# Performance work log

Measured on AMD Instinct MI355X. Metric: run time of the kernel, lower is better.

## Reference

```python
import jax, jax.numpy as jnp
import numpy as np

B, LC, LM, D = 128, 512, 512, 512

def setup_inputs() -> dict:
    key = jax.random.key(0)
    k1, k2, k3 = jax.random.split(key, 3)
    context = jax.random.normal(k1, (B, LC, D), dtype=jnp.float32)
    main = jax.random.normal(k2, (B, LM, D), dtype=jnp.float32)
    W = jax.random.normal(k3, (D, 1), dtype=jnp.float32)
    return {"context": context, "main": main, "W": W}

def reference(context, main, W):
    # scores[b,c,m] = <context[b,c,:], main[b,m,:]>
    scores = jnp.einsum('bcd,bmd->bcm', context, main)
    # softmax over last axis (main positions), matching K.softmax default axis=-1
    attn = jax.nn.softmax(scores, axis=-1)           # [B, LC, LM]
    # Keras dot(axes=1): contract context-position axis -> [B, LM, D]
    aligned = jnp.einsum('bcm,bcd->bmd', attn, context)
    diff = main - aligned                            # [B, LM, D]
    # project to scalar per main position, softmax over positions
    w = jax.nn.softmax(jnp.einsum('bmd,d->bm', diff, W[:, 0]), axis=-1)  # [B, LM]
    # weighted sum over main positions -> [B, D]
    out = jnp.einsum('bm,bmd->bd', w, diff)
    return out
```

## Files before the change

kernel.cpp:

```cpp
#include <hip/hip_runtime.h>

#define B_  128
#define LC_ 512
#define LM_ 512
#define D_  512

typedef __attribute__((ext_vector_type(8))) short short8;
typedef __attribute__((ext_vector_type(16))) float f32x16;
typedef unsigned int u32;

__device__ __forceinline__ unsigned short bf16_rn(float x) {
  unsigned u = __float_as_uint(x);
  unsigned r = u + 0x7fffu + ((u >> 16) & 1u);
  return (unsigned short)(r >> 16);
}
__device__ __forceinline__ float bf2f(short s) {
  return __uint_as_float((u32)(unsigned short)s << 16);
}
__device__ __forceinline__ void gl_lds16(const void* g, void* l) {
  __builtin_amdgcn_global_load_lds((const __attribute__((address_space(1))) u32*)g,
                                   (__attribute__((address_space(3))) u32*)l, 16, 0, 0);
}

#define CVT1(SRC, WS, AH, AL, IDX, ACCU)                         \
  { unsigned short hb_ = bf16_rn(SRC);                           \
    float hf_ = __uint_as_float((u32)hb_ << 16);                 \
    AH[IDX] = (short)hb_;                                        \
    AL[IDX] = (short)bf16_rn((SRC) - hf_);                       \
    ACCU = fmaf((SRC), (WS), ACCU); }

__global__ __launch_bounds__(256) void k_cvt_main(
    const float* __restrict__ mn, const float* __restrict__ W,
    short* __restrict__ BtH, short* __restrict__ BtL,
    float* __restrict__ v) {
  __shared__ float sW[512];
  int tid = threadIdx.x;
  sW[tid] = W[tid];
  sW[tid + 256] = W[tid + 256];
  __syncthreads();
  int wave = blockIdx.x * 4 + (tid >> 6);
  int b = wave >> 4, mt = wave & 15;
  int lane = tid & 63, rowl = lane & 31, h = lane >> 5;
  const float* src = mn + ((size_t)b * LM_ + 32 * mt + rowl) * D_ + 8 * h;
  float acc = 0.f;
  for (int ks = 0; ks < 32; ks++) {
    float4 f0 = *(const float4*)(src + 16 * ks);
    float4 f1 = *(const float4*)(src + 16 * ks + 4);
    int k = 16 * ks + 8 * h;
    float4 w0 = *(const float4*)&sW[k];
    float4 w1 = *(const float4*)&sW[k + 4];
    short8 vh, vl;
    CVT1(f0.x, w0.x, vh, vl, 0, acc); CVT1(f0.y, w0.y, vh, vl, 1, acc);
    CVT1(f0.z, w0.z, vh, vl, 2, acc); CVT1(f0.w, w0.w, vh, vl, 3, acc);
    CVT1(f1.x, w1.x, vh, vl, 4, acc); CVT1(f1.y, w1.y, vh, vl, 5, acc);
    CVT1(f1.z, w1.z, vh, vl, 6, acc); CVT1(f1.w, w1.w, vh, vl, 7, acc);
    size_t off = (((size_t)b * 32 + ks) * 16 + mt) * 512 + (size_t)lane * 8;
    *(short8*)(BtH + off) = vh;
    *(short8*)(BtL + off) = vl;
  }
  acc += __shfl_xor(acc, 32, 64);
  if (h == 0) v[b * LM_ + 32 * mt + rowl] = acc;
}

struct __align__(16) Smem3 {
  short8 Bf[2][2][16][64];
  short8 Af[2][2][4][64];
  float sW[512];
  float red[4][128];
  float cmb[128];
  float uld[128];
  float tpw[2][4][128];
};

__global__ __launch_bounds__(512, 2) void k_scores_mfma9(
    const float* __restrict__ ctx, const short* __restrict__ BtH,
    const short* __restrict__ BtL, const float* __restrict__ W,
    unsigned short* __restrict__ P16, float* __restrict__ tpart) {
  __shared__ Smem3 sm;
  int p = blockIdx.x;
  int b = (p & 7) | ((p >> 5) << 3);
  int cblk = (p >> 3) & 3;
  int c0 = cblk * 128;
  int tid = threadIdx.x;
  int lane = tid & 63, wv = tid >> 6;
  int rowl = lane & 31, h = lane >> 5;

  f32x16 acc[2][4];
  #pragma unroll
  for (int r = 0; r < 2; r++)
    #pragma unroll
    for (int mtl = 0; mtl < 4; mtl++)
      #pragma unroll
      for (int j = 0; j < 16; j++) acc[r][mtl][j] = 0.f;

  auto stageB = [&](int bf, int ks) {
    #pragma unroll
    for (int rep = 0; rep < 2; rep++) {
      int mt = wv + 8 * rep;
      size_t off = (((size_t)b * 32 + ks) * 16 + mt) * 512 + (size_t)lane * 8;
      gl_lds16(BtH + off, &sm.Bf[bf][0][mt][0]);
      gl_lds16(BtL + off, &sm.Bf[bf][1][mt][0]);
    }
  };
  auto cvtA = [&](int bf, int ks, const float4& g0, const float4& g1, float& au) {
    float xs[8] = {g0.x, g0.y, g0.z, g0.w, g1.x, g1.y, g1.z, g1.w};
    int k = 16 * ks + 8 * h;
    float4 w0 = *(const float4*)&sm.sW[k];
    float4 w1 = *(const float4*)&sm.sW[k + 4];
    float ws[8] = {w0.x, w0.y, w0.z, w0.w, w1.x, w1.y, w1.z, w1.w};
    short8 vh, vl;
    #pragma unroll
    for (int e = 0; e < 8; e++) {
      unsigned short hb = bf16_rn(xs[e]);
      float hf = __uint_as_float((unsigned)hb << 16);
      vh[e] = (short)hb;
      vl[e] = (short)bf16_rn(xs[e] - hf);
      au = fmaf(xs[e], ws[e], au);
    }
    *(short8*)&sm.Af[bf][0][wv][lane] = vh;
    *(short8*)&sm.Af[bf][1][wv][lane] = vl;
  };

  sm.sW[tid] = W[tid];
  float accu = 0.f;
  stageB(0, 0);
  const float* arow = ctx + ((size_t)b * LC_ + c0 + 32 * wv + rowl) * D_ + 8 * h;
  float4 g0, g1;
  if (wv < 4) {
    g0 = *(const float4*)(arow);
    g1 = *(const float4*)(arow + 4);
  }
  __syncthreads();
  if (wv < 4) cvtA(0, 0, g0, g1, accu);
  __syncthreads();

  for (int ks = 0; ks < 32; ks++) {
    int buf = ks & 1;
    if (ks < 31) {
      stageB(buf ^ 1, ks + 1);
      if (wv < 4) {
        const float* ap = arow + 16 * (ks + 1);
        g0 = *(const float4*)ap;
        g1 = *(const float4*)(ap + 4);
      }
    }
    int rt0 = (wv >> 2) * 2;
    short8 ah0 = sm.Af[buf][0][rt0][lane];
    short8 ah1 = sm.Af[buf][0][rt0 + 1][lane];
    short8 al0 = sm.Af[buf][1][rt0][lane];
    short8 al1 = sm.Af[buf][1][rt0 + 1][lane];
    #pragma unroll
    for (int mtl = 0; mtl < 4; mtl++) {
      int mtg = (wv & 3) * 4 + mtl;
      short8 bh = sm.Bf[buf][0][mtg][lane];
      short8 bl = sm.Bf[buf][1][mtg][lane];
      acc[0][mtl] = __builtin_amdgcn_mfma_f32_32x32x16_bf16(ah0, bh, acc[0][mtl], 0, 0, 0);
      acc[0][mtl] = __builtin_amdgcn_mfma_f32_32x32x16_bf16(ah0, bl, acc[0][mtl], 0, 0, 0);
      acc[0][mtl] = __builtin_amdgcn_mfma_f32_32x32x16_bf16(al0, bh, acc[0][mtl], 0, 0, 0);
      acc[1][mtl] = __builtin_amdgcn_mfma_f32_32x32x16_bf16(ah1, bh, acc[1][mtl], 0, 0, 0);
      acc[1][mtl] = __builtin_amdgcn_mfma_f32_32x32x16_bf16(ah1, bl, acc[1][mtl], 0, 0, 0);
      acc[1][mtl] = __builtin_amdgcn_mfma_f32_32x32x16_bf16(al1, bh, acc[1][mtl], 0, 0, 0);
    }
    if (ks < 31 && wv < 4) cvtA(buf ^ 1, ks + 1, g0, g1, accu);
    __syncthreads();
  }

  if (wv < 4) {
    accu += __shfl_xor(accu, 32, 64);
    if (h == 0) sm.uld[32 * wv + rowl] = accu;
  }

  #pragma unroll
  for (int r = 0; r < 2; r++)
    #pragma unroll
    for (int j = 0; j < 16; j++) {
      float mx = fmaxf(fmaxf(acc[r][0][j], acc[r][1][j]),
                       fmaxf(acc[r][2][j], acc[r][3][j]));
      #pragma unroll
      for (int s = 1; s <= 16; s <<= 1) mx = fmaxf(mx, __shfl_xor(mx, s, 64));
      if (rowl == 0)
        sm.red[wv & 3][64 * (wv >> 2) + 32 * r + (j & 3) + 8 * (j >> 2) + 4 * h] = mx;
    }
  __syncthreads();
  if (tid < 128)
    sm.cmb[tid] = fmaxf(fmaxf(sm.red[0][tid], sm.red[1][tid]),
                        fmaxf(sm.red[2][tid], sm.red[3][tid]));
  __syncthreads();
  #pragma unroll
  for (int r = 0; r < 2; r++)
    #pragma unroll
    for (int j = 0; j < 16; j++) {
      int row = 64 * (wv >> 2) + 32 * r + (j & 3) + 8 * (j >> 2) + 4 * h;
      float mx = sm.cmb[row];
      float s = 0.f;
      #pragma unroll
      for (int mtl = 0; mtl < 4; mtl++) {
        float e = __expf(acc[r][mtl][j] - mx);
        acc[r][mtl][j] = e;
        s += e;
      }
      #pragma unroll
      for (int st = 1; st <= 16; st <<= 1) s += __shfl_xor(s, st, 64);
      if (rowl == 0) sm.red[wv & 3][row] = s;
    }
  __syncthreads();
  if (tid < 128)
    sm.cmb[tid] = sm.red[0][tid] + sm.red[1][tid] + sm.red[2][tid] + sm.red[3][tid];
  __syncthreads();

  unsigned short* Pb = P16 + ((size_t)b * LC_ + c0) * LM_;
  float tp[4] = {0.f, 0.f, 0.f, 0.f};
  #pragma unroll
  for (int r = 0; r < 2; r++)
    #pragma unroll
    for (int j = 0; j < 16; j++) {
      int row = 64 * (wv >> 2) + 32 * r + (j & 3) + 8 * (j >> 2) + 4 * h;
      float rinv = 1.f / sm.cmb[row];
      float uu = sm.uld[row];
      #pragma unroll
      for (int mtl = 0; mtl < 4; mtl++) {
        float pv = acc[r][mtl][j] * rinv;
        Pb[(size_t)row * LM_ + 128 * (wv & 3) + 32 * mtl + rowl] = bf16_rn(pv);
        tp[mtl] = fmaf(pv, uu, tp[mtl]);
      }
    }
  #pragma unroll
  for (int mtl = 0; mtl < 4; mtl++) tp[mtl] += __shfl_xor(tp[mtl], 32, 64);
  if (h == 0) {
    #pragma unroll
    for (int mtl = 0; mtl < 4; mtl++)
      sm.tpw[wv >> 2][wv & 3][32 * mtl + rowl] = tp[mtl];
  }
  __syncthreads();
  {
    int m = tid;
    tpart[((size_t)b * 4 + cblk) * LM_ + m] =
        sm.tpw[0][m >> 7][m & 127] + sm.tpw[1][m >> 7][m & 127];
  }
}

__global__ __launch_bounds__(256) void k_tw(const float* __restrict__ tpart,
                                            const float* __restrict__ v,
                                            float* __restrict__ w_) {
  int b = blockIdx.x;
  int tid = threadIdx.x;
  int m0 = tid * 2;
  const float* tp = tpart + (size_t)b * 4 * LM_;
  float s0 = 0.f, s1 = 0.f;
  #pragma unroll
  for (int cb = 0; cb < 4; cb++) {
    s0 += tp[cb * LM_ + m0];
    s1 += tp[cb * LM_ + m0 + 1];
  }
  float x0 = v[b * LM_ + m0] - s0;
  float x1 = v[b * LM_ + m0 + 1] - s1;
  float mx = fmaxf(x0, x1);
  #pragma unroll
  for (int s = 32; s >= 1; s >>= 1) mx = fmaxf(mx, __shfl_xor(mx, s, 64));
  __shared__ float redm[4], reds[4];
  int wvv = tid >> 6, ln = tid & 63;
  if (ln == 0) redm[wvv] = mx;
  __syncthreads();
  mx = fmaxf(fmaxf(redm[0], redm[1]), fmaxf(redm[2], redm[3]));
  float e0 = __expf(x0 - mx), e1 = __expf(x1 - mx);
  float sum = e0 + e1;
  #pragma unroll
  for (int s = 32; s >= 1; s >>= 1) sum += __shfl_xor(sum, s, 64);
  if (ln == 0) reds[wvv] = sum;
  __syncthreads();
  sum = reds[0] + reds[1] + reds[2] + reds[3];
  float rinv = 1.0f / sum;
  float2 o; o.x = e0 * rinv; o.y = e1 * rinv;
  *(float2*)&w_[b * LM_ + m0] = o;
}

__global__ __launch_bounds__(256) void k_q(const unsigned short* __restrict__ P16,
                                           const float* __restrict__ w,
                                           float* __restrict__ q) {
  int b = blockIdx.y;
  int c0 = blockIdx.x * 32;
  int wvv = threadIdx.x >> 6, ln = threadIdx.x & 63;
  __shared__ float sw[LM_];
  *(float2*)&sw[threadIdx.x * 2] = *(const float2*)&w[b * LM_ + threadIdx.x * 2];
  __syncthreads();
  #pragma unroll
  for (int rr = 0; rr < 8; rr++) {
    int c = c0 + wvv * 8 + rr;
    short8 pv = *((const short8*)(P16 + ((size_t)b * LC_ + c) * LM_) + ln);
    float4 w0 = *(const float4*)&sw[ln * 8];
    float4 w1 = *(const float4*)&sw[ln * 8 + 4];
    float acc = bf2f(pv[0]) * w0.x + bf2f(pv[1]) * w0.y
              + bf2f(pv[2]) * w0.z + bf2f(pv[3]) * w0.w
              + bf2f(pv[4]) * w1.x + bf2f(pv[5]) * w1.y
              + bf2f(pv[6]) * w1.z + bf2f(pv[7]) * w1.w;
    #pragma unroll
    for (int s = 32; s >= 1; s >>= 1) acc += __shfl_xor(acc, s, 64);
    if (ln == 0) q[b * LC_ + c] = acc;
  }
}

__global__ __launch_bounds__(256) void k_out(const float* __restrict__ ctx,
                                             const short* __restrict__ BtH,
                                             const short* __restrict__ BtL,
                                             const float* __restrict__ w,
                                             const float* __restrict__ q,
                                             float* __restrict__ out) {
  int b = blockIdx.y;
  int d0 = blockIdx.x * 64;
  int ks0 = d0 >> 4;
  int tid = threadIdx.x;
  int lane = tid & 63, wvv = tid >> 6;
  int rowl = lane & 31, h = lane >> 5;
  __shared__ float sw_[LM_];
  __shared__ float redo[4][64];
  __shared__ float red2[4][64];
  sw_[tid] = w[b * LM_ + tid];
  sw_[tid + 256] = w[b * LM_ + tid + 256];
  __syncthreads();

  float mp[4][8];
  #pragma unroll
  for (int ksl = 0; ksl < 4; ksl++)
    #pragma unroll
    for (int e = 0; e < 8; e++) mp[ksl][e] = 0.f;
  for (int mt = wvv; mt < 16; mt += 4) {
    float wm = sw_[32 * mt + rowl];
    #pragma unroll
    for (int ksl = 0; ksl < 4; ksl++) {
      size_t off = (((size_t)b * 32 + ks0 + ksl) * 16 + mt) * 512 + (size_t)lane * 8;
      short8 hh = *(const short8*)(BtH + off);
      short8 ll = *(const short8*)(BtL + off);
      #pragma unroll
      for (int e = 0; e < 8; e++)
        mp[ksl][e] = fmaf(wm, bf2f(hh[e]) + bf2f(ll[e]), mp[ksl][e]);
    }
  }
  #pragma unroll
  for (int ksl = 0; ksl < 4; ksl++)
    #pragma unroll
    for (int e = 0; e < 8; e++) {
      float vsum = mp[ksl][e];
      #pragma unroll
      for (int s = 1; s <= 16; s <<= 1) vsum += __shfl_xor(vsum, s, 64);
      mp[ksl][e] = vsum;
    }
  if (rowl == 0) {
    #pragma unroll
    for (int ksl = 0; ksl < 4; ksl++)
      #pragma unroll
      for (int e = 0; e < 8; e++)
        redo[wvv][16 * ksl + 8 * h + e] = mp[ksl][e];
  }

  int td = tid & 63;
  int tg = tid >> 6;
  const float* Cb = ctx + (size_t)b * LC_ * D_ + d0;
  const float* qb = q + b * LC_;
  float acc = 0.f;
  #pragma unroll 4
  for (int c = tg; c < LC_; c += 4) acc -= qb[c] * Cb[(size_t)c * D_ + td];
  red2[tg][td] = acc;
  __syncthreads();
  if (tg == 0)
    out[b * D_ + d0 + td] =
        redo[0][td] + redo[1][td] + redo[2][td] + redo[3][td] +
        red2[0][td] + red2[1][td] + red2[2][td] + red2[3][td];
}

extern "C" void kernel_launch(void* const* d_in, const int* in_sizes, int n_in,
                              void* d_out, int out_size, void* d_ws, size_t ws_size,
                              hipStream_t stream) {
  const float* ctx = (const float*)d_in[0];
  const float* mn  = (const float*)d_in[1];
  const float* W   = (const float*)d_in[2];
  float* out = (float*)d_out;

  char* base = (char*)d_ws;
  size_t nP16   = (size_t)B_ * LC_ * LM_ * 2;
  size_t planeB = (size_t)B_ * LM_ * D_ * 2;

  unsigned short* P16 = (unsigned short*)base;
  short* BtH = (short*)(base + nP16);
  short* BtL = (short*)(base + nP16 + planeB);
  char* p2 = base + nP16 + 2 * planeB;
  float* tpart = (float*)p2;  p2 += (size_t)B_ * 4 * LM_ * 4;
  float* v = (float*)p2;      p2 += (size_t)B_ * LM_ * 4;
  float* w = (float*)p2;      p2 += (size_t)B_ * LM_ * 4;
  float* q = (float*)p2;

  k_cvt_main<<<dim3(512), 256, 0, stream>>>(mn, W, BtH, BtL, v);
  k_scores_mfma9<<<dim3(512), 512, 0, stream>>>(ctx, BtH, BtL, W, P16, tpart);
  k_tw<<<dim3(B_), 256, 0, stream>>>(tpart, v, w);
  k_q<<<dim3(LC_ / 32, B_), 256, 0, stream>>>(P16, w, q);
  k_out<<<dim3(D_ / 64, B_), 256, 0, stream>>>(ctx, BtH, BtL, w, q, out);
}
```

Baseline: 255.5 us.

## Split scores kernel across 16 waves with one m-tile per wave

The scores kernel now launches 1024 threads (16 waves) per block instead of 512. Each wave owns a single 32-column m-tile across all four row tiles instead of two row tiles by four m-tiles. Softmax reductions combine 16 per-wave partials, and each wave writes its tpart column directly, which drops the tpw staging buffer and one barrier. The aim is more waves in flight to hide latency and a simpler epilogue. The cost is that the A fragments are now read from LDS by all 16 waves, and the launch bound no longer requests 2 blocks per CU.

```diff
diff --git a/kernel.cpp b/kernel.cpp
--- a/kernel.cpp
+++ b/kernel.cpp
@@ -62,21 +62,20 @@
   if (h == 0) v[b * LM_ + 32 * mt + rowl] = acc;
 }
 
-struct __align__(16) Smem3 {
+struct __align__(16) Smem10 {
   short8 Bf[2][2][16][64];
   short8 Af[2][2][4][64];
   float sW[512];
-  float red[4][128];
+  float red[16][128];
   float cmb[128];
   float uld[128];
-  float tpw[2][4][128];
 };
 
-__global__ __launch_bounds__(512, 2) void k_scores_mfma9(
+__global__ __launch_bounds__(1024) void k_scores_mfma10(
     const float* __restrict__ ctx, const short* __restrict__ BtH,
     const short* __restrict__ BtL, const float* __restrict__ W,
     unsigned short* __restrict__ P16, float* __restrict__ tpart) {
-  __shared__ Smem3 sm;
+  __shared__ Smem10 sm;
   int p = blockIdx.x;
   int b = (p & 7) | ((p >> 5) << 3);
   int cblk = (p >> 3) & 3;
@@ -85,22 +84,16 @@
   int lane = tid & 63, wv = tid >> 6;
   int rowl = lane & 31, h = lane >> 5;
 
-  f32x16 acc[2][4];
-  #pragma unroll
-  for (int r = 0; r < 2; r++)
-    #pragma unroll
-    for (int mtl = 0; mtl < 4; mtl++)
-      #pragma unroll
-      for (int j = 0; j < 16; j++) acc[r][mtl][j] = 0.f;
+  f32x16 acc[4];
+  #pragma unroll
+  for (int rt = 0; rt < 4; rt++)
+    #pragma unroll
+    for (int j = 0; j < 16; j++) acc[rt][j] = 0.f;
 
   auto stageB = [&](int bf, int ks) {
-    #pragma unroll
-    for (int rep = 0; rep < 2; rep++) {
-      int mt = wv + 8 * rep;
-      size_t off = (((size_t)b * 32 + ks) * 16 + mt) * 512 + (size_t)lane * 8;
-      gl_lds16(BtH + off, &sm.Bf[bf][0][mt][0]);
-      gl_lds16(BtL + off, &sm.Bf[bf][1][mt][0]);
-    }
+    size_t off = (((size_t)b * 32 + ks) * 16 + wv) * 512 + (size_t)lane * 8;
+    gl_lds16(BtH + off, &sm.Bf[bf][0][wv][0]);
+    gl_lds16(BtL + off, &sm.Bf[bf][1][wv][0]);
   };
   auto cvtA = [&](int bf, int ks, const float4& g0, const float4& g1, float& au) {
     float xs[8] = {g0.x, g0.y, g0.z, g0.w, g1.x, g1.y, g1.z, g1.w};
@@ -121,7 +114,7 @@
     *(short8*)&sm.Af[bf][1][wv][lane] = vl;
   };
 
-  sm.sW[tid] = W[tid];
+  if (tid < 512) sm.sW[tid] = W[tid];
   float accu = 0.f;
   stageB(0, 0);
   const float* arow = ctx + ((size_t)b * LC_ + c0 + 32 * wv + rowl) * D_ + 8 * h;
@@ -144,22 +137,15 @@
         g1 = *(const float4*)(ap + 4);
       }
     }
-    int rt0 = (wv >> 2) * 2;
-    short8 ah0 = sm.Af[buf][0][rt0][lane];
-    short8 ah1 = sm.Af[buf][0][rt0 + 1][lane];
-    short8 al0 = sm.Af[buf][1][rt0][lane];
-    short8 al1 = sm.Af[buf][1][rt0 + 1][lane];
-    #pragma unroll
-    for (int mtl = 0; mtl < 4; mtl++) {
-      int mtg = (wv & 3) * 4 + mtl;
-      short8 bh = sm.Bf[buf][0][mtg][lane];
-      short8 bl = sm.Bf[buf][1][mtg][lane];
-      acc[0][mtl] = __builtin_amdgcn_mfma_f32_32x32x16_bf16(ah0, bh, acc[0][mtl], 0, 0, 0);
-      acc[0][mtl] = __builtin_amdgcn_mfma_f32_32x32x16_bf16(ah0, bl, acc[0][mtl], 0, 0, 0);
-      acc[0][mtl] = __builtin_amdgcn_mfma_f32_32x32x16_bf16(al0, bh, acc[0][mtl], 0, 0, 0);
-      acc[1][mtl] = __builtin_amdgcn_mfma_f32_32x32x16_bf16(ah1, bh, acc[1][mtl], 0, 0, 0);
-      acc[1][mtl] = __builtin_amdgcn_mfma_f32_32x32x16_bf16(ah1, bl, acc[1][mtl], 0, 0, 0);
-      acc[1][mtl] = __builtin_amdgcn_mfma_f32_32x32x16_bf16(al1, bh, acc[1][mtl], 0, 0, 0);
+    short8 bh = sm.Bf[buf][0][wv][lane];
+    short8 bl = sm.Bf[buf][1][wv][lane];
+    #pragma unroll
+    for (int rt = 0; rt < 4; rt++) {
+      short8 ah = sm.Af[buf][0][rt][lane];
+      short8 al = sm.Af[buf][1][rt][lane];
+      acc[rt] = __builtin_amdgcn_mfma_f32_32x32x16_bf16(ah, bh, acc[rt], 0, 0, 0);
+      acc[rt] = __builtin_amdgcn_mfma_f32_32x32x16_bf16(ah, bl, acc[rt], 0, 0, 0);
+      acc[rt] = __builtin_amdgcn_mfma_f32_32x32x16_bf16(al, bh, acc[rt], 0, 0, 0);
     }
     if (ks < 31 && wv < 4) cvtA(buf ^ 1, ks + 1, g0, g1, accu);
     __syncthreads();
@@ -171,72 +157,59 @@
   }
 
   #pragma unroll
-  for (int r = 0; r < 2; r++)
+  for (int rt = 0; rt < 4; rt++)
     #pragma unroll
     for (int j = 0; j < 16; j++) {
-      float mx = fmaxf(fmaxf(acc[r][0][j], acc[r][1][j]),
-                       fmaxf(acc[r][2][j], acc[r][3][j]));
+      float mx = acc[rt][j];
       #pragma unroll
       for (int s = 1; s <= 16; s <<= 1) mx = fmaxf(mx, __shfl_xor(mx, s, 64));
       if (rowl == 0)
-        sm.red[wv & 3][64 * (wv >> 2) + 32 * r + (j & 3) + 8 * (j >> 2) + 4 * h] = mx;
-    }
-  __syncthreads();
-  if (tid < 128)
-    sm.cmb[tid] = fmaxf(fmaxf(sm.red[0][tid], sm.red[1][tid]),
-                        fmaxf(sm.red[2][tid], sm.red[3][tid]));
-  __syncthreads();
-  #pragma unroll
-  for (int r = 0; r < 2; r++)
+        sm.red[wv][32 * rt + (j & 3) + 8 * (j >> 2) + 4 * h] = mx;
+    }
+  __syncthreads();
+  if (tid < 128) {
+    float m0 = sm.red[0][tid];
+    #pragma unroll
+    for (int w2 = 1; w2 < 16; w2++) m0 = fmaxf(m0, sm.red[w2][tid]);
+    sm.cmb[tid] = m0;
+  }
+  __syncthreads();
+  #pragma unroll
+  for (int rt = 0; rt < 4; rt++)
     #pragma unroll
     for (int j = 0; j < 16; j++) {
-      int row = 64 * (wv >> 2) + 32 * r + (j & 3) + 8 * (j >> 2) + 4 * h;
-      float mx = sm.cmb[row];
-      float s = 0.f;
-      #pragma unroll
-      for (int mtl = 0; mtl < 4; mtl++) {
-        float e = __expf(acc[r][mtl][j] - mx);
-        acc[r][mtl][j] = e;
-        s += e;
-      }
+      int row = 32 * rt + (j & 3) + 8 * (j >> 2) + 4 * h;
+      float e = __expf(acc[rt][j] - sm.cmb[row]);
+      acc[rt][j] = e;
+      float s = e;
       #pragma unroll
       for (int st = 1; st <= 16; st <<= 1) s += __shfl_xor(s, st, 64);
-      if (rowl == 0) sm.red[wv & 3][row] = s;
-    }
-  __syncthreads();
-  if (tid < 128)
-    sm.cmb[tid] = sm.red[0][tid] + sm.red[1][tid] + sm.red[2][tid] + sm.red[3][tid];
+      if (rowl == 0) sm.red[wv][row] = s;
+    }
+  __syncthreads();
+  if (tid < 128) {
+    float s0 = sm.red[0][tid];
+    #pragma unroll
+    for (int w2 = 1; w2 < 16; w2++) s0 += sm.red[w2][tid];
+    sm.cmb[tid] = s0;
+  }
   __syncthreads();
 
   unsigned short* Pb = P16 + ((size_t)b * LC_ + c0) * LM_;
-  float tp[4] = {0.f, 0.f, 0.f, 0.f};
-  #pragma unroll
-  for (int r = 0; r < 2; r++)
+  float tp = 0.f;
+  int col = 32 * wv + rowl;
+  #pragma unroll
+  for (int rt = 0; rt < 4; rt++)
     #pragma unroll
     for (int j = 0; j < 16; j++) {
-      int row = 64 * (wv >> 2) + 32 * r + (j & 3) + 8 * (j >> 2) + 4 * h;
-      float rinv = 1.f / sm.cmb[row];
-      float uu = sm.uld[row];
-      #pragma unroll
-      for (int mtl = 0; mtl < 4; mtl++) {
-        float pv = acc[r][mtl][j] * rinv;
-        Pb[(size_t)row * LM_ + 128 * (wv & 3) + 32 * mtl + rowl] = bf16_rn(pv);
-        tp[mtl] = fmaf(pv, uu, tp[mtl]);
-      }
-    }
-  #pragma unroll
-  for (int mtl = 0; mtl < 4; mtl++) tp[mtl] += __shfl_xor(tp[mtl], 32, 64);
-  if (h == 0) {
-    #pragma unroll
-    for (int mtl = 0; mtl < 4; mtl++)
-      sm.tpw[wv >> 2][wv & 3][32 * mtl + rowl] = tp[mtl];
-  }
-  __syncthreads();
-  {
-    int m = tid;
-    tpart[((size_t)b * 4 + cblk) * LM_ + m] =
-        sm.tpw[0][m >> 7][m & 127] + sm.tpw[1][m >> 7][m & 127];
-  }
+      int row = 32 * rt + (j & 3) + 8 * (j >> 2) + 4 * h;
+      float pv = acc[rt][j] * (1.f / sm.cmb[row]);
+      Pb[(size_t)row * LM_ + col] = bf16_rn(pv);
+      tp = fmaf(pv, sm.uld[row], tp);
+    }
+  tp += __shfl_xor(tp, 32, 64);
+  if (h == 0)
+    tpart[((size_t)b * 4 + cblk) * LM_ + col] = tp;
 }
 
 __global__ __launch_bounds__(256) void k_tw(const float* __restrict__ tpart,
@@ -389,7 +362,7 @@
   float* q = (float*)p2;
 
   k_cvt_main<<<dim3(512), 256, 0, stream>>>(mn, W, BtH, BtL, v);
-  k_scores_mfma9<<<dim3(512), 512, 0, stream>>>(ctx, BtH, BtL, W, P16, tpart);
+  k_scores_mfma10<<<dim3(512), 1024, 0, stream>>>(ctx, BtH, BtL, W, P16, tpart);
   k_tw<<<dim3(B_), 256, 0, stream>>>(tpart, v, w);
   k_q<<<dim3(LC_ / 32, B_), 256, 0, stream>>>(P16, w, q);
   k_out<<<dim3(D_ / 64, B_), 256, 0, stream>>>(ctx, BtH, BtL, w, q, out);
```

After: 312.4 us. 1.22x slower.
